# Optimization experiments

Measured on AMD Instinct MI355X. Metric: run time of the kernel, lower is better.

The kernel has to match this reference:

```python
import jax, jax.numpy as jnp
import numpy as np

B, S, HID = 1, 4096, 2048
H, KVH, D = 8, 4, 256
SW = 1024          # sliding window
EPS = 1e-6
NEG = -1e30


def _rmsnorm(x, w=None, eps=EPS):
    # torch nn.RMSNorm: x / sqrt(mean(x^2) + eps) * weight
    y = x * jax.lax.rsqrt(jnp.mean(x * x, axis=-1, keepdims=True) + eps)
    return y * w if w is not None else y


def _rotate_half(x):
    x1, x2 = jnp.split(x, 2, axis=-1)
    return jnp.concatenate([-x2, x1], axis=-1)


def _rope(x, cos, sin):
    # x: [B,S,H,D]; cos/sin: [B,S,rot] -> [B,S,1,rot]; rot == D here (no pass-through)
    c = cos[:, :, None, :]
    s = sin[:, :, None, :]
    return x * c + _rotate_half(x) * s


def setup_inputs() -> dict:
    key = jax.random.key(0)
    ks = jax.random.split(key, 9)
    return {
        "hidden_states": jax.random.normal(ks[0], (B, S, HID), jnp.float32),
        "cos": jax.random.uniform(ks[1], (B, S, D), jnp.float32),
        "sin": jax.random.uniform(ks[2], (B, S, D), jnp.float32),
        "q_w": jax.random.normal(ks[3], (H * D, HID), jnp.float32) * 0.02,
        "k_w": jax.random.normal(ks[4], (KVH * D, HID), jnp.float32) * 0.02,
        "v_w": jax.random.normal(ks[5], (KVH * D, HID), jnp.float32) * 0.02,
        "o_w": jax.random.normal(ks[6], (HID, H * D), jnp.float32) * 0.02,
        "q_norm_w": jnp.ones((D,), jnp.float32),
        "k_norm_w": jnp.ones((D,), jnp.float32),
    }


def reference(hidden_states, cos, sin, q_w, k_w, v_w, o_w, q_norm_w, k_norm_w):
    b, s, _ = hidden_states.shape
    # Projections (no bias), reshape to [B,S,heads,D]
    q = (hidden_states @ q_w.T).reshape(b, s, H, D)
    k = (hidden_states @ k_w.T).reshape(b, s, KVH, D)
    v = (hidden_states @ v_w.T).reshape(b, s, KVH, D)
    # per-head RMSNorm (v_norm has no affine), then RoPE on q/k
    q = _rope(_rmsnorm(q, q_norm_w), cos, sin)
    k = _rope(_rmsnorm(k, k_norm_w), cos, sin)
    v = _rmsnorm(v)
    # flatten(0,1): packed tokens T = B*S
    T = b * s
    q = q.reshape(T, H, D).transpose(1, 0, 2)          # [H,T,D]
    k = k.reshape(T, KVH, D).transpose(1, 0, 2)        # [KVH,T,D]
    v = v.reshape(T, KVH, D).transpose(1, 0, 2)
    # GQA: repeat_interleave kv heads
    rep = H // KVH
    k = jnp.repeat(k, rep, axis=0)                     # [H,T,D]
    v = jnp.repeat(v, rep, axis=0)
    # causal + sliding-window mask (allowed: i-SW < j <= i), scale=1.0
    i = jnp.arange(T)[:, None]
    j = jnp.arange(T)[None, :]
    allowed = (j <= i) & ((i - j) < SW)                # [T,T] bool
    scores = jnp.einsum("htd,hsd->hts", q, k)          # [H,T,T]
    scores = jnp.where(allowed[None], scores, NEG)
    p = jax.nn.softmax(scores, axis=-1)
    out = jnp.einsum("hts,hsd->htd", p, v)             # [H,T,D]
    out = out.transpose(1, 0, 2).reshape(b, s, H * D)
    return out @ o_w.T
```

## Files before the change

### kernel.cpp

```cpp
#include <hip/hip_runtime.h>
#include <stdint.h>

typedef __bf16 bf16x8 __attribute__((ext_vector_type(8)));
typedef __bf16 bf16x4 __attribute__((ext_vector_type(4)));
typedef float f32x4v __attribute__((ext_vector_type(4)));

__device__ __forceinline__ void async_copy16(const void* gptr, void* ldsptr) {
  __builtin_amdgcn_global_load_lds(
      (const __attribute__((address_space(1))) void*)gptr,
      (__attribute__((address_space(3))) void*)ldsptr,
      16, 0, 0);
}

__global__ __launch_bounds__(256) void cvt_split(
    const float* __restrict__ src, __bf16* __restrict__ hi,
    __bf16* __restrict__ lo, int n4) {
  const int i = blockIdx.x * 256 + threadIdx.x;
  if (i < n4) {
    const float4 v = ((const float4*)src)[i];
    float vv[4] = {v.x, v.y, v.z, v.w};
    bf16x4 h, l;
    for (int j = 0; j < 4; ++j) {
      h[j] = (__bf16)vv[j];
      l[j] = (__bf16)(vv[j] - (float)h[j]);
    }
    ((bf16x4*)hi)[i] = h;
    ((bf16x4*)lo)[i] = l;
  }
}

__global__ __launch_bounds__(256, 3) void gemm_qkv(
    const __bf16* __restrict__ Ah, const __bf16* __restrict__ Al,
    const __bf16* __restrict__ Bh, const __bf16* __restrict__ Bl,
    float* __restrict__ C) {
  const int K = 2048, ldc = 4096;
  __shared__ __align__(16) __bf16 Ash[128 * 32];
  __shared__ __align__(16) __bf16 Asl[128 * 32];
  __shared__ __align__(16) __bf16 Bsh[128 * 32];
  __shared__ __align__(16) __bf16 Bsl[128 * 32];
  const int bid = blockIdx.x;
  const int xcd = bid & 7, c = bid >> 3;
  const int m0 = (c >> 2) * 128, n0 = (xcd * 4 + (c & 3)) * 128;
  const int tid = threadIdx.x;
  const int wid = tid >> 6, lane = tid & 63, l15 = lane & 15, quad = lane >> 4;
  const int wm = wid >> 1, wn = wid & 1;

  f32x4v acc[4][4] = {};

  for (int kb = 0; kb < K; kb += 32) {
    for (int it = 0; it < 2; ++it) {
      const int cc = (wid * 2 + it) * 64 + lane;
      const int row = cc >> 2;
      const int sc = (cc & 3) ^ (row & 3);
      const size_t ao = (size_t)(m0 + row) * K + kb + sc * 8;
      const size_t bo = (size_t)(n0 + row) * K + kb + sc * 8;
      const int dst = (wid * 2 + it) * 512;
      async_copy16(Ah + ao, &Ash[dst]);
      async_copy16(Al + ao, &Asl[dst]);
      async_copy16(Bh + bo, &Bsh[dst]);
      async_copy16(Bl + bo, &Bsl[dst]);
    }
    __syncthreads();
    bf16x8 afh[4], afl[4], bfh[4], bfl[4];
    for (int mt = 0; mt < 4; ++mt) {
      const int r = wm * 64 + mt * 16 + l15;
      const int o = r * 32 + ((quad ^ (r & 3)) * 8);
      afh[mt] = *(const bf16x8*)&Ash[o];
      afl[mt] = *(const bf16x8*)&Asl[o];
    }
    for (int nt = 0; nt < 4; ++nt) {
      const int r = wn * 64 + nt * 16 + l15;
      const int o = r * 32 + ((quad ^ (r & 3)) * 8);
      bfh[nt] = *(const bf16x8*)&Bsh[o];
      bfl[nt] = *(const bf16x8*)&Bsl[o];
    }
    for (int mt = 0; mt < 4; ++mt)
      for (int nt = 0; nt < 4; ++nt) {
        acc[mt][nt] = __builtin_amdgcn_mfma_f32_16x16x32_bf16(afh[mt], bfh[nt], acc[mt][nt], 0, 0, 0);
        acc[mt][nt] = __builtin_amdgcn_mfma_f32_16x16x32_bf16(afh[mt], bfl[nt], acc[mt][nt], 0, 0, 0);
        acc[mt][nt] = __builtin_amdgcn_mfma_f32_16x16x32_bf16(afl[mt], bfh[nt], acc[mt][nt], 0, 0, 0);
      }
    __syncthreads();
  }
  for (int mt = 0; mt < 4; ++mt)
    for (int nt = 0; nt < 4; ++nt) {
      const int row = m0 + wm * 64 + mt * 16 + quad * 4;
      const int col = n0 + wn * 64 + nt * 16 + l15;
      for (int r = 0; r < 4; ++r)
        C[(size_t)(row + r) * ldc + col] = acc[mt][nt][r];
    }
}

__global__ __launch_bounds__(64) void norm_rope(
    const float* __restrict__ qkv, const float* __restrict__ cosb,
    const float* __restrict__ sinb, const float* __restrict__ qnw,
    const float* __restrict__ knw,
    __bf16* __restrict__ qh, __bf16* __restrict__ ql,
    __bf16* __restrict__ kh, __bf16* __restrict__ kl,
    __bf16* __restrict__ vT) {
  const int s = blockIdx.x, c = blockIdx.y, lane = threadIdx.x;
  const int d0 = lane * 4;
  const float4 xv = *(const float4*)(qkv + (size_t)s * 4096 + c * 256 + d0);
  float v[4] = {xv.x, xv.y, xv.z, xv.w};
  float ss = v[0] * v[0] + v[1] * v[1] + v[2] * v[2] + v[3] * v[3];
  for (int off = 1; off < 64; off <<= 1) ss += __shfl_xor(ss, off);
  const float rn = rsqrtf(ss * (1.0f / 256.0f) + 1e-6f);
  if (c < 12) {
    const float* w = (c < 8) ? qnw : knw;
    float y[4], yp[4];
    for (int j = 0; j < 4; ++j) y[j] = v[j] * rn * w[d0 + j];
    for (int j = 0; j < 4; ++j) yp[j] = __shfl_xor(y[j], 32);
    for (int j = 0; j < 4; ++j) {
      const int d = d0 + j;
      const float rot = (d < 128) ? -yp[j] : yp[j];
      y[j] = y[j] * cosb[s * 256 + d] + rot * sinb[s * 256 + d];
    }
    const size_t o = (c < 8) ? ((size_t)c * 4096 + s) * 256 + d0
                             : ((size_t)(c - 8) * 4096 + s) * 256 + d0;
    __bf16* dh = (c < 8) ? qh : kh;
    __bf16* dl = (c < 8) ? ql : kl;
    bf16x4 hv, lv;
    for (int j = 0; j < 4; ++j) {
      hv[j] = (__bf16)y[j];
      lv[j] = (__bf16)(y[j] - (float)hv[j]);
    }
    *(bf16x4*)(dh + o) = hv;
    *(bf16x4*)(dl + o) = lv;
  } else {
    const int kvh = c - 12;
    for (int j = 0; j < 4; ++j)
      vT[(size_t)(kvh * 256 + d0 + j) * 4096 + s] = (__bf16)(v[j] * rn);
  }
}

__global__ __launch_bounds__(512, 2) void attn_mfma(
    const __bf16* __restrict__ Qh_, const __bf16* __restrict__ Ql_,
    const __bf16* __restrict__ Kh_, const __bf16* __restrict__ Kl_,
    const __bf16* __restrict__ VT, __bf16* __restrict__ Aout) {
  const int S = 4096, D = 256;
  const int bid = blockIdx.y * 32 + blockIdx.x;
  const int swz = (bid & 7) * 32 + (bid >> 3);
  const int h = swz >> 5;
  const int q0 = (swz & 31) * 128;
  const int tid = threadIdx.x;
  const int wid = tid >> 6, lane = tid & 63, l15 = lane & 15, quad = lane >> 4;
  const int kv = h >> 1;

  __shared__ __align__(16) __bf16 Ksh[2][32 * 256];
  __shared__ __align__(16) __bf16 Ksl[2][32 * 256];
  __shared__ __align__(16) __bf16 Vs[2][256 * 32];
  __shared__ __align__(16) __bf16 P[8][16][32];

  const __bf16* Khh = Kh_ + (size_t)kv * S * D;
  const __bf16* Khl = Kl_ + (size_t)kv * S * D;
  const __bf16* Vh = VT + (size_t)kv * D * S;

  auto stage = [&](int buf, int kt) {
    for (int set = 0; set < 2; ++set) {
      const int n = set * 512 + wid * 64 + lane;
      const int row = n >> 5, c = n & 31;
      const int sc = c ^ (row & 7);
      const size_t go = (size_t)(kt + row) * D + sc * 8;
      const int dst = (set * 512 + wid * 64) * 8;
      async_copy16(Khh + go, &Ksh[buf][dst]);
      async_copy16(Khl + go, &Ksl[buf][dst]);
      const int dim = n >> 2, kc = n & 3;
      const size_t vo = (size_t)dim * S + kt + kc * 8;
      async_copy16(Vh + vo, &Vs[buf][dst]);
    }
  };

  bf16x8 qfh[8], qfl[8];
  {
    const size_t qoff =
        (size_t)h * S * D + (size_t)(q0 + wid * 16 + l15) * D + quad * 8;
    for (int ks = 0; ks < 8; ++ks) {
      qfh[ks] = *(const bf16x8*)(Qh_ + qoff + ks * 32);
      qfl[ks] = *(const bf16x8*)(Ql_ + qoff + ks * 32);
    }
  }

  f32x4v O[16] = {};
  float mrow[4] = {-1e30f, -1e30f, -1e30f, -1e30f};
  float lrow[4] = {0.f, 0.f, 0.f, 0.f};

  const int lo = (q0 >= 1024) ? (q0 - 1024) : 0;
  const int hi = q0 + 96;
  const int iqmin = q0 + wid * 16;
  const int iqmax = iqmin + 15;

  stage(0, lo);
  __syncthreads();
  int cur = 0;

  for (int kt = lo; kt <= hi; kt += 32) {
    if (kt + 32 <= hi) stage(cur ^ 1, kt + 32);
    const bool active = (kt <= iqmax) && (kt + 31 >= iqmin - 1023);
    if (active) {
      f32x4v sa[2] = {};
      for (int nt = 0; nt < 2; ++nt) {
        const int row = nt * 16 + l15;
        const int rxk = row & 7;
        for (int ks = 0; ks < 8; ++ks) {
          const int c = (ks * 4 + quad) ^ rxk;
          const bf16x8 kh8 = *(const bf16x8*)&Ksh[cur][row * 256 + c * 8];
          const bf16x8 kl8 = *(const bf16x8*)&Ksl[cur][row * 256 + c * 8];
          sa[nt] = __builtin_amdgcn_mfma_f32_16x16x32_bf16(qfh[ks], kh8, sa[nt], 0, 0, 0);
          sa[nt] = __builtin_amdgcn_mfma_f32_16x16x32_bf16(qfh[ks], kl8, sa[nt], 0, 0, 0);
          sa[nt] = __builtin_amdgcn_mfma_f32_16x16x32_bf16(qfl[ks], kh8, sa[nt], 0, 0, 0);
        }
      }
      float al[4];
      for (int r = 0; r < 4; ++r) {
        const int i = q0 + wid * 16 + quad * 4 + r;
        float mx = -1e30f;
        for (int nt = 0; nt < 2; ++nt) {
          const int j = kt + nt * 16 + l15;
          const float svv = ((j <= i) && (i - j < 1024)) ? sa[nt][r] : -1e30f;
          sa[nt][r] = svv;
          mx = fmaxf(mx, svv);
        }
        for (int off = 1; off < 16; off <<= 1) mx = fmaxf(mx, __shfl_xor(mx, off));
        const float mn = fmaxf(mrow[r], mx);
        al[r] = __expf(mrow[r] - mn);
        float ps = 0.f;
        for (int nt = 0; nt < 2; ++nt) {
          const float p = (mn <= -1e29f) ? 0.f : __expf(sa[nt][r] - mn);
          P[wid][quad * 4 + r][nt * 16 + l15] = (__bf16)p;
          ps += p;
        }
        for (int off = 1; off < 16; off <<= 1) ps += __shfl_xor(ps, off);
        lrow[r] = lrow[r] * al[r] + ps;
        mrow[r] = mn;
      }
      for (int nt2 = 0; nt2 < 16; ++nt2)
        for (int r = 0; r < 4; ++r) O[nt2][r] *= al[r];
      __asm__ volatile("s_waitcnt lgkmcnt(0)" ::: "memory");
      __builtin_amdgcn_sched_barrier(0);
      const bf16x8 pf = *(const bf16x8*)&P[wid][l15][quad * 8];
      for (int nt2 = 0; nt2 < 16; ++nt2) {
        const int dim = nt2 * 16 + l15;
        const bf16x8 vf = *(const bf16x8*)&Vs[cur][(dim * 4 + quad) * 8];
        O[nt2] = __builtin_amdgcn_mfma_f32_16x16x32_bf16(pf, vf, O[nt2], 0, 0, 0);
      }
    }
    __syncthreads();
    cur ^= 1;
  }
  for (int nt2 = 0; nt2 < 16; ++nt2)
    for (int r = 0; r < 4; ++r) {
      const float o = O[nt2][r] / lrow[r];
      Aout[(size_t)(q0 + wid * 16 + quad * 4 + r) * 2048 + h * 256 + nt2 * 16 + l15] = (__bf16)o;
    }
}

__global__ __launch_bounds__(256, 2) void gemm_out(
    const __bf16* __restrict__ A, const float* __restrict__ B,
    float* __restrict__ C) {
  const int K = 2048, ldc = 2048;
  __shared__ __align__(16) __bf16 As[128 * 32];
  __shared__ __align__(16) __bf16 Bs[128 * 32];
  const int m0 = blockIdx.y * 128, n0 = blockIdx.x * 128;
  const int tid = threadIdx.x;
  const int wid = tid >> 6, lane = tid & 63, l15 = lane & 15, quad = lane >> 4;
  const int wm = wid >> 1, wn = wid & 1;

  f32x4v acc[4][4] = {};

  for (int kb = 0; kb < K; kb += 32) {
    for (int cc = 0; cc < 2; ++cc) {
      const int c = cc * 256 + tid;
      const int row = c >> 2, col = (c & 3) * 8;
      *(bf16x8*)&As[row * 32 + col] =
          *(const bf16x8*)(A + (size_t)(m0 + row) * K + kb + col);
    }
    for (int cc = 0; cc < 4; ++cc) {
      const int c = cc * 256 + tid;
      const int row = c >> 3, col = (c & 7) * 4;
      const float4 bv = *(const float4*)(B + (size_t)(n0 + row) * K + kb + col);
      bf16x4 bh = {(__bf16)bv.x, (__bf16)bv.y, (__bf16)bv.z, (__bf16)bv.w};
      *(bf16x4*)&Bs[row * 32 + col] = bh;
    }
    __syncthreads();
    bf16x8 af[4], bfr[4];
    for (int mt = 0; mt < 4; ++mt)
      af[mt] = *(const bf16x8*)&As[(wm * 64 + mt * 16 + l15) * 32 + quad * 8];
    for (int nt = 0; nt < 4; ++nt)
      bfr[nt] = *(const bf16x8*)&Bs[(wn * 64 + nt * 16 + l15) * 32 + quad * 8];
    for (int mt = 0; mt < 4; ++mt)
      for (int nt = 0; nt < 4; ++nt)
        acc[mt][nt] = __builtin_amdgcn_mfma_f32_16x16x32_bf16(af[mt], bfr[nt], acc[mt][nt], 0, 0, 0);
    __syncthreads();
  }
  for (int mt = 0; mt < 4; ++mt)
    for (int nt = 0; nt < 4; ++nt) {
      const int row = m0 + wm * 64 + mt * 16 + quad * 4;
      const int col = n0 + wn * 64 + nt * 16 + l15;
      for (int r = 0; r < 4; ++r)
        C[(size_t)(row + r) * ldc + col] = acc[mt][nt][r];
    }
}

extern "C" void kernel_launch(void* const* d_in, const int* in_sizes, int n_in,
                              void* d_out, int out_size, void* d_ws, size_t ws_size,
                              hipStream_t stream) {
  const float* hidden = (const float*)d_in[0];
  const float* cosb   = (const float*)d_in[1];
  const float* sinb   = (const float*)d_in[2];
  const float* qw     = (const float*)d_in[3];
  const float* kw     = (const float*)d_in[4];
  const float* vw     = (const float*)d_in[5];
  const float* ow     = (const float*)d_in[6];
  const float* qnw    = (const float*)d_in[7];
  const float* knw    = (const float*)d_in[8];
  float* out = (float*)d_out;

  const size_t MB = 1048576;
  char* ws = (char*)d_ws;
  float*  qkvf = (float*)ws;
  __bf16* attn = (__bf16*)ws;
  __bf16* hh   = (__bf16*)(ws + 64 * MB);
  __bf16* hl   = (__bf16*)(ws + 80 * MB);
  __bf16* wh   = (__bf16*)(ws + 96 * MB);
  __bf16* wl   = (__bf16*)(ws + 112 * MB);
  __bf16* qh   = (__bf16*)(ws + 64 * MB);
  __bf16* ql   = (__bf16*)(ws + 80 * MB);
  __bf16* kh   = (__bf16*)(ws + 96 * MB);
  __bf16* kl   = (__bf16*)(ws + 104 * MB);
  __bf16* vT   = (__bf16*)(ws + 112 * MB);

  cvt_split<<<dim3(8192), 256, 0, stream>>>(hidden, hh, hl, 2097152);
  cvt_split<<<dim3(4096), 256, 0, stream>>>(qw, wh, wl, 1048576);
  cvt_split<<<dim3(2048), 256, 0, stream>>>(kw, wh + 4194304, wl + 4194304, 524288);
  cvt_split<<<dim3(2048), 256, 0, stream>>>(vw, wh + 6291456, wl + 6291456, 524288);

  gemm_qkv<<<dim3(1024), 256, 0, stream>>>(hh, hl, wh, wl, qkvf);
  norm_rope<<<dim3(4096, 16), 64, 0, stream>>>(qkvf, cosb, sinb, qnw, knw,
                                               qh, ql, kh, kl, vT);
  attn_mfma<<<dim3(32, 8), 512, 0, stream>>>(qh, ql, kh, kl, vT, attn);
  gemm_out<<<dim3(16, 32), 256, 0, stream>>>(attn, ow, out);
}
```

Baseline: 573.6 us.

## Double-buffer QKV GEMM LDS tiles and fix LDS bank-conflict swizzles

The QKV projection GEMM now keeps two LDS stages and prefetches the next K-slice with async global-to-LDS copies while computing on the current one, so load latency overlaps with the MFMA work. The launch-bounds occupancy drops from 3 to 2 blocks per CU to make room for the doubled shared memory. The XOR swizzle on A/B tiles changes to use (row>>1)&3, and new swizzles are added to the attention kernel's V tile and P scratch buffer, all aimed at reducing LDS bank conflicts on the 16-byte reads. The visible GEMM loop no longer shows its leading barrier, so correctness depends on a barrier after the compute before the buffer is overwritten.

After: 599.1 us. 4.4% more time.

```diff
diff --git a/kernel.cpp b/kernel.cpp
--- a/kernel.cpp
+++ b/kernel.cpp
@@ -29,15 +29,15 @@
   }
 }
 
-__global__ __launch_bounds__(256, 3) void gemm_qkv(
+__global__ __launch_bounds__(256, 2) void gemm_qkv(
     const __bf16* __restrict__ Ah, const __bf16* __restrict__ Al,
     const __bf16* __restrict__ Bh, const __bf16* __restrict__ Bl,
     float* __restrict__ C) {
   const int K = 2048, ldc = 4096;
-  __shared__ __align__(16) __bf16 Ash[128 * 32];
-  __shared__ __align__(16) __bf16 Asl[128 * 32];
-  __shared__ __align__(16) __bf16 Bsh[128 * 32];
-  __shared__ __align__(16) __bf16 Bsl[128 * 32];
+  __shared__ __align__(16) __bf16 Ash[2][128 * 32];
+  __shared__ __align__(16) __bf16 Asl[2][128 * 32];
+  __shared__ __align__(16) __bf16 Bsh[2][128 * 32];
+  __shared__ __align__(16) __bf16 Bsl[2][128 * 32];
   const int bid = blockIdx.x;
   const int xcd = bid & 7, c = bid >> 3;
   const int m0 = (c >> 2) * 128, n0 = (xcd * 4 + (c & 3)) * 128;
@@ -47,32 +47,39 @@
 
   f32x4v acc[4][4] = {};
 
-  for (int kb = 0; kb < K; kb += 32) {
+  auto stage = [&](int buf, int kb) {
     for (int it = 0; it < 2; ++it) {
       const int cc = (wid * 2 + it) * 64 + lane;
       const int row = cc >> 2;
-      const int sc = (cc & 3) ^ (row & 3);
+      const int sc = (cc & 3) ^ ((row >> 1) & 3);
       const size_t ao = (size_t)(m0 + row) * K + kb + sc * 8;
       const size_t bo = (size_t)(n0 + row) * K + kb + sc * 8;
       const int dst = (wid * 2 + it) * 512;
-      async_copy16(Ah + ao, &Ash[dst]);
-      async_copy16(Al + ao, &Asl[dst]);
-      async_copy16(Bh + bo, &Bsh[dst]);
-      async_copy16(Bl + bo, &Bsl[dst]);
-    }
-    __syncthreads();
+      async_copy16(Ah + ao, &Ash[buf][dst]);
+      async_copy16(Al + ao, &Asl[buf][dst]);
+      async_copy16(Bh + bo, &Bsh[buf][dst]);
+      async_copy16(Bl + bo, &Bsl[buf][dst]);
+    }
+  };
+
+  stage(0, 0);
+  __syncthreads();
+
+  for (int t = 0; t < 64; ++t) {
+    const int buf = t & 1;
+    if (t < 63) stage(buf ^ 1, (t + 1) * 32);
     bf16x8 afh[4], afl[4], bfh[4], bfl[4];
     for (int mt = 0; mt < 4; ++mt) {
       const int r = wm * 64 + mt * 16 + l15;
-      const int o = r * 32 + ((quad ^ (r & 3)) * 8);
-      afh[mt] = *(const bf16x8*)&Ash[o];
-      afl[mt] = *(const bf16x8*)&Asl[o];
+      const int o = r * 32 + ((quad ^ ((r >> 1) & 3)) * 8);
+      afh[mt] = *(const bf16x8*)&Ash[buf][o];
+      afl[mt] = *(const bf16x8*)&Asl[buf][o];
     }
     for (int nt = 0; nt < 4; ++nt) {
       const int r = wn * 64 + nt * 16 + l15;
-      const int o = r * 32 + ((quad ^ (r & 3)) * 8);
-      bfh[nt] = *(const bf16x8*)&Bsh[o];
-      bfl[nt] = *(const bf16x8*)&Bsl[o];
+      const int o = r * 32 + ((quad ^ ((r >> 1) & 3)) * 8);
+      bfh[nt] = *(const bf16x8*)&Bsh[buf][o];
+      bfl[nt] = *(const bf16x8*)&Bsl[buf][o];
     }
     for (int mt = 0; mt < 4; ++mt)
       for (int nt = 0; nt < 4; ++nt) {
@@ -165,7 +172,7 @@
       async_copy16(Khh + go, &Ksh[buf][dst]);
       async_copy16(Khl + go, &Ksl[buf][dst]);
       const int dim = n >> 2, kc = n & 3;
-      const size_t vo = (size_t)dim * S + kt + kc * 8;
+      const size_t vo = (size_t)dim * S + kt + (kc ^ ((dim >> 1) & 3)) * 8;
       async_copy16(Vh + vo, &Vs[buf][dst]);
     }
   };
@@ -224,9 +231,12 @@
         const float mn = fmaxf(mrow[r], mx);
         al[r] = __expf(mrow[r] - mn);
         float ps = 0.f;
+        const int prow = quad * 4 + r;
+        const int px = (prow >> 1) & 3;
         for (int nt = 0; nt < 2; ++nt) {
           const float p = (mn <= -1e29f) ? 0.f : __expf(sa[nt][r] - mn);
-          P[wid][quad * 4 + r][nt * 16 + l15] = (__bf16)p;
+          const int pc = (nt * 2 + (l15 >> 3)) ^ px;
+          P[wid][prow][pc * 8 + (l15 & 7)] = (__bf16)p;
           ps += p;
         }
         for (int off = 1; off < 16; off <<= 1) ps += __shfl_xor(ps, off);
@@ -237,10 +247,12 @@
         for (int r = 0; r < 4; ++r) O[nt2][r] *= al[r];
       __asm__ volatile("s_waitcnt lgkmcnt(0)" ::: "memory");
       __builtin_amdgcn_sched_barrier(0);
-      const bf16x8 pf = *(const bf16x8*)&P[wid][l15][quad * 8];
+      const int prx = (l15 >> 1) & 3;
+      const bf16x8 pf = *(const bf16x8*)&P[wid][l15][(quad ^ prx) * 8];
       for (int nt2 = 0; nt2 < 16; ++nt2) {
         const int dim = nt2 * 16 + l15;
-        const bf16x8 vf = *(const bf16x8*)&Vs[cur][(dim * 4 + quad) * 8];
+        const int vq = quad ^ ((dim >> 1) & 3);
+        const bf16x8 vf = *(const bf16x8*)&Vs[cur][(dim * 4 + vq) * 8];
         O[nt2] = __builtin_amdgcn_mfma_f32_16x16x32_bf16(pf, vf, O[nt2], 0, 0, 0);
       }
     }
```
